# Performance work log

Hardware: AMD Instinct MI355X
Metric: run time of the kernel (lower is better)

Reference implementation:

```python
import jax, jax.numpy as jnp
import numpy as np

TARGET_SPARSITY = 0.9
LN_EPS = 1e-5


def ternary_quant(W):
    """BitNet-b1.58 style ternary quantization: W -> {-1,0,+1} * mean(|W|).
    Straight-through estimator so gradients pass to the latent weights."""
    scale = jnp.mean(jnp.abs(W))
    q = jnp.clip(jnp.round(W / (scale + 1e-8)), -1.0, 1.0) * scale
    return W + jax.lax.stop_gradient(q - W)


def layernorm(x, gamma, beta):
    mu = jnp.mean(x, axis=-1, keepdims=True)
    var = jnp.var(x, axis=-1, keepdims=True)
    return (x - mu) * jax.lax.rsqrt(var + LN_EPS) * gamma + beta


def setup_inputs() -> dict:
    key = jax.random.key(0)
    ks = jax.random.split(key, 3)
    B, S, D, N = 4, 2048, 2048, 8192
    x = jax.random.normal(ks[0], (B, S, D), dtype=jnp.float32)
    W_syn = jax.random.normal(ks[1], (N, D), dtype=jnp.float32) * (1.0 / np.sqrt(D))
    b_syn = jnp.zeros((N,), dtype=jnp.float32)
    W_out = jax.random.normal(ks[2], (D, N), dtype=jnp.float32) * (1.0 / np.sqrt(N))
    b_out = jnp.zeros((D,), dtype=jnp.float32)
    gamma = jnp.ones((D,), dtype=jnp.float32)
    beta = jnp.zeros((D,), dtype=jnp.float32)
    return {"x": x, "W_syn": W_syn, "b_syn": b_syn, "W_out": W_out,
            "b_out": b_out, "gamma": gamma, "beta": beta}


def reference(x, W_syn, b_syn, W_out, b_out, gamma, beta):
    B, S, D = x.shape
    N = W_syn.shape[0]
    x_flat = x.reshape(-1, D)  # [T, D], T = B*S

    # RNU: ternary-weight synapses + sparse firing (keep top (1-sparsity) per token)
    z = x_flat @ ternary_quant(W_syn).T + b_syn  # [T, N]
    k = max(1, int(N * (1.0 - TARGET_SPARSITY)))
    topv, _ = jax.lax.top_k(z, k)                 # [T, k]
    thresh = topv[:, -1:]                          # k-th largest per token
    hidden = jnp.where(z >= thresh, jax.nn.relu(z), 0.0)  # sparse firing rates

    # Ternary output projection
    out = hidden @ ternary_quant(W_out).T + b_out  # [T, D]
    out = out.reshape(B, S, D)

    # Residual + LayerNorm
    return layernorm(x + out, gamma, beta)
```

## Files before the change

kernel.cpp:

```cpp
#include <hip/hip_runtime.h>


typedef __attribute__((ext_vector_type(8))) short short8;
typedef __attribute__((ext_vector_type(4))) float f32x4;

__device__ __forceinline__ float bf2f(unsigned h) {
    return __uint_as_float(h << 16);
}
__device__ __forceinline__ unsigned f2bf(float f) {
    unsigned u = __float_as_uint(f);
    return (u + 0x7fffu + ((u >> 16) & 1u)) >> 16;
}

typedef __attribute__((address_space(1))) const void gq_void;
typedef __attribute__((address_space(3))) void ls_void;
__device__ __forceinline__ void gload16(const void* g, void* l) {
    __builtin_amdgcn_global_load_lds((gq_void*)g, (ls_void*)l, 16, 0, 0);
}

#define CFENCE() asm volatile("" ::: "memory")
#define BARRIER()                    \
    do {                             \
        CFENCE();                    \
        __builtin_amdgcn_s_barrier(); \
        CFENCE();                    \
    } while (0)

__global__ __launch_bounds__(64) void init_detect(float* sc, const unsigned* g_raw,
                                                  int* flag) {
    if (threadIdx.x < 16) sc[threadIdx.x] = 0.0f;
    if (threadIdx.x == 0) *flag = (g_raw[0] == 0x3F803F80u) ? 1 : 0;
}

__global__ __launch_bounds__(256) void split_x(const void* __restrict__ src,
                                               unsigned short* __restrict__ hi,
                                               unsigned short* __restrict__ lo, int n,
                                               const int* __restrict__ flagp) {
    const int flag = *flagp;
    int idx = blockIdx.x * 256 + threadIdx.x;
    int stride = gridDim.x * 256;
    if (flag) {
        const uint4* s = (const uint4*)src;
        uint4* dh = (uint4*)hi;
        uint4* dl = (uint4*)lo;
        uint4 zz; zz.x = zz.y = zz.z = zz.w = 0u;
        for (int i = idx; i < n / 8; i += stride) { dh[i] = s[i]; dl[i] = zz; }
    } else {
        const float4* s = (const float4*)src;
        uint2* dh = (uint2*)hi;
        uint2* dl = (uint2*)lo;
        for (int i = idx; i < n / 4; i += stride) {
            float4 v = s[i];
            unsigned h0 = f2bf(v.x), h1 = f2bf(v.y), h2 = f2bf(v.z), h3 = f2bf(v.w);
            unsigned l0 = f2bf(v.x - bf2f(h0));
            unsigned l1 = f2bf(v.y - bf2f(h1));
            unsigned l2 = f2bf(v.z - bf2f(h2));
            unsigned l3 = f2bf(v.w - bf2f(h3));
            uint2 oh; oh.x = h0 | (h1 << 16); oh.y = h2 | (h3 << 16);
            uint2 ol; ol.x = l0 | (l1 << 16); ol.y = l2 | (l3 << 16);
            dh[i] = oh;
            dl[i] = ol;
        }
    }
}

__global__ __launch_bounds__(256) void to_f32(const void* __restrict__ src,
                                              float* __restrict__ dst, int n,
                                              const int* __restrict__ flagp) {
    const int flag = *flagp;
    int i = blockIdx.x * 256 + threadIdx.x;
    if (i >= n) return;
    if (flag) dst[i] = bf2f((unsigned)((const unsigned short*)src)[i]);
    else dst[i] = ((const float*)src)[i];
}

__global__ __launch_bounds__(256) void abs_sum_any(const void* __restrict__ w, int n,
                                                   float* __restrict__ out,
                                                   const int* __restrict__ flagp) {
    const int flag = *flagp;
    int idx = blockIdx.x * 256 + threadIdx.x;
    int stride = gridDim.x * 256;
    float s = 0.0f;
    if (flag) {
        const uint4* wv = (const uint4*)w;
        for (int c = idx; c < n / 8; c += stride) {
            uint4 v = wv[c];
            unsigned a[4] = {v.x, v.y, v.z, v.w};
#pragma unroll
            for (int j = 0; j < 4; j++)
                s += fabsf(bf2f(a[j] & 0xffffu)) + fabsf(bf2f(a[j] >> 16));
        }
    } else {
        const float4* wv = (const float4*)w;
        for (int c = idx; c < n / 4; c += stride) {
            float4 v = wv[c];
            s += fabsf(v.x) + fabsf(v.y) + fabsf(v.z) + fabsf(v.w);
        }
    }
#pragma unroll
    for (int off = 32; off; off >>= 1) s += __shfl_down(s, off);
    __shared__ float red[4];
    int lane = threadIdx.x & 63, wv_id = threadIdx.x >> 6;
    if (lane == 0) red[wv_id] = s;
    __syncthreads();
    if (threadIdx.x == 0) atomicAdd(out, red[0] + red[1] + red[2] + red[3]);
}

__global__ __launch_bounds__(64) void finalize_scale(float* sc, float inv_count) {
    if (threadIdx.x == 0) {
        sc[2] = sc[0] * inv_count;
        sc[3] = sc[1] * inv_count;
    }
}

__global__ __launch_bounds__(256) void quantize_any(const void* __restrict__ w,
                                                    unsigned short* __restrict__ q,
                                                    const float* __restrict__ sc, int idx,
                                                    int n, const int* __restrict__ flagp) {
    const int flag = *flagp;
    const float d = sc[idx] + 1e-8f;
    int i = blockIdx.x * 256 + threadIdx.x;
    int stride = gridDim.x * 256;
    if (flag) {
        const uint4* wv = (const uint4*)w;
        uint4* qv = (uint4*)q;
        for (; i < n / 8; i += stride) {
            uint4 v = wv[i];
            unsigned a[4] = {v.x, v.y, v.z, v.w};
            unsigned r[4];
#pragma unroll
            for (int j = 0; j < 4; j++) {
                float lo = bf2f(a[j] & 0xffffu);
                float hi = bf2f(a[j] >> 16);
                float rl = fminf(1.0f, fmaxf(-1.0f, rintf(lo / d)));
                float rh = fminf(1.0f, fmaxf(-1.0f, rintf(hi / d)));
                r[j] = f2bf(rl) | (f2bf(rh) << 16);
            }
            uint4 o;
            o.x = r[0]; o.y = r[1]; o.z = r[2]; o.w = r[3];
            qv[i] = o;
        }
    } else {
        const float4* wv = (const float4*)w;
        uint2* qv = (uint2*)q;
        for (; i < n / 4; i += stride) {
            float4 v = wv[i];
            float r0 = fminf(1.0f, fmaxf(-1.0f, rintf(v.x / d)));
            float r1 = fminf(1.0f, fmaxf(-1.0f, rintf(v.y / d)));
            float r2 = fminf(1.0f, fmaxf(-1.0f, rintf(v.z / d)));
            float r3 = fminf(1.0f, fmaxf(-1.0f, rintf(v.w / d)));
            uint2 o;
            o.x = f2bf(r0) | (f2bf(r1) << 16);
            o.y = f2bf(r2) | (f2bf(r3) << 16);
            qv[i] = o;
        }
    }
}

template <bool DUAL_A>
__global__ __launch_bounds__(512, 2) void gemm8p(const unsigned short* __restrict__ A0,
                                                 const unsigned short* __restrict__ A1,
                                                 const unsigned short* __restrict__ B,
                                                 float* __restrict__ C,
                                                 const float* __restrict__ biasf,
                                                 const float* __restrict__ scp,
                                                 int scidx, int N, int K) {
    __shared__ uint4 L4[8192];

    const int tid = threadIdx.x;
    const int lane = tid & 63;
    const int wave = tid >> 6;
    const int wr = wave >> 2;
    const int wc = wave & 3;
    const int l15 = lane & 15;
    const int quad = lane >> 4;

    const int nwg = gridDim.x * gridDim.y;
    int orig = blockIdx.y * gridDim.x + blockIdx.x;
    int id = orig;
    if ((nwg & 7) == 0) id = (orig & 7) * (nwg >> 3) + (orig >> 3);
    const int bx = id % gridDim.x;
    const int by = id / gridDim.x;
    const int m0 = by * 256;
    const int n0 = bx * 256;

    f32x4 acc[8][4];
#pragma unroll
    for (int i = 0; i < 8; i++)
#pragma unroll
        for (int j = 0; j < 4; j++) acc[i][j] = (f32x4){0.f, 0.f, 0.f, 0.f};

    const unsigned short* Apan0 = A0 + (size_t)m0 * K;
    const unsigned short* Apan1 = DUAL_A ? (A1 + (size_t)m0 * K) : nullptr;
    const unsigned short* Bpan = B + (size_t)n0 * K;

    const int NT = DUAL_A ? (K >> 5) : (K >> 6);

    auto stage = [&](const unsigned short* g, int kcol, int dstChunkBase) {
#pragma unroll
        for (int i = 0; i < 2; i++) {
            int pc = tid + i * 512;
            int r = pc >> 2;
            int c4 = (pc & 3) ^ (r & 3);
            gload16(g + (size_t)r * K + kcol + c4 * 8,
                    L4 + dstChunkBase + (tid & 448) + i * 512);
        }
    };
    auto dstA = [&](int b, int s) { return (b * 2 + s) * 1024; };
    auto dstB = [&](int b, int s) { return 4096 + (b * 2 + s) * 1024; };

    auto rdA = [&](int b, int s, int R) -> short8 {
        return *(const short8*)(L4 + (b * 2 + s) * 1024 + R * 4 + (quad ^ (R & 3)));
    };
    auto rdB = [&](int b, int s, int R) -> short8 {
        return *(const short8*)(L4 + 4096 + (b * 2 + s) * 1024 + R * 4 +
                                (quad ^ (R & 3)));
    };

    stage(Apan0, 0, dstA(0, 0));
    stage(Bpan, 0, dstB(0, 0));
    stage(Apan0, 32, dstA(0, 1));
    stage(Bpan, 32, dstB(0, 1));
    asm volatile("s_waitcnt vmcnt(4)" ::: "memory");
    BARRIER();

    for (int t = 0; t < NT; ++t) {
        const int b = t & 1;
        const int bn = b ^ 1;
        const bool st = (t + 1 < NT);
        const unsigned short* Anext =
            (DUAL_A && ((t + 1) & 1)) ? Apan1 : Apan0;
        const int kbn = DUAL_A ? (((t + 1) >> 1) << 6) : ((t + 1) << 6);

        short8 a[8], b0, b1;

#pragma unroll
        for (int m = 0; m < 8; m++) a[m] = rdA(b, 0, wr * 128 + m * 16 + l15);
        b0 = rdB(b, 0, wc * 64 + 0 + l15);
        b1 = rdB(b, 0, wc * 64 + 16 + l15);
        if (st) stage(Anext, kbn + 0, dstA(bn, 0));
        BARRIER();
        __builtin_amdgcn_s_setprio(1);
#pragma unroll
        for (int m = 0; m < 8; m++) {
            acc[m][0] = __builtin_amdgcn_mfma_f32_16x16x32_bf16(a[m], b0, acc[m][0], 0, 0, 0);
            acc[m][1] = __builtin_amdgcn_mfma_f32_16x16x32_bf16(a[m], b1, acc[m][1], 0, 0, 0);
        }
        __builtin_amdgcn_s_setprio(0);
        BARRIER();

        b0 = rdB(b, 0, wc * 64 + 32 + l15);
        b1 = rdB(b, 0, wc * 64 + 48 + l15);
        if (st) {
            stage(Bpan, kbn + 0, dstB(bn, 0));
            asm volatile("s_waitcnt vmcnt(4)" ::: "memory");
        } else {
            asm volatile("s_waitcnt vmcnt(0)" ::: "memory");
        }
        BARRIER();
        __builtin_amdgcn_s_setprio(1);
#pragma unroll
        for (int m = 0; m < 8; m++) {
            acc[m][2] = __builtin_amdgcn_mfma_f32_16x16x32_bf16(a[m], b0, acc[m][2], 0, 0, 0);
            acc[m][3] = __builtin_amdgcn_mfma_f32_16x16x32_bf16(a[m], b1, acc[m][3], 0, 0, 0);
        }
        __builtin_amdgcn_s_setprio(0);
        BARRIER();

#pragma unroll
        for (int m = 0; m < 8; m++) a[m] = rdA(b, 1, wr * 128 + m * 16 + l15);
        b0 = rdB(b, 1, wc * 64 + 0 + l15);
        b1 = rdB(b, 1, wc * 64 + 16 + l15);
        if (st) stage(Anext, kbn + 32, dstA(bn, 1));
        BARRIER();
        __builtin_amdgcn_s_setprio(1);
#pragma unroll
        for (int m = 0; m < 8; m++) {
            acc[m][0] = __builtin_amdgcn_mfma_f32_16x16x32_bf16(a[m], b0, acc[m][0], 0, 0, 0);
            acc[m][1] = __builtin_amdgcn_mfma_f32_16x16x32_bf16(a[m], b1, acc[m][1], 0, 0, 0);
        }
        __builtin_amdgcn_s_setprio(0);
        BARRIER();

        b0 = rdB(b, 1, wc * 64 + 32 + l15);
        b1 = rdB(b, 1, wc * 64 + 48 + l15);
        if (st) {
            stage(Bpan, kbn + 32, dstB(bn, 1));
            asm volatile("s_waitcnt vmcnt(4)" ::: "memory");
        }
        BARRIER();
        __builtin_amdgcn_s_setprio(1);
#pragma unroll
        for (int m = 0; m < 8; m++) {
            acc[m][2] = __builtin_amdgcn_mfma_f32_16x16x32_bf16(a[m], b0, acc[m][2], 0, 0, 0);
            acc[m][3] = __builtin_amdgcn_mfma_f32_16x16x32_bf16(a[m], b1, acc[m][3], 0, 0, 0);
        }
        __builtin_amdgcn_s_setprio(0);
        BARRIER();
    }

    const float scale = scp[scidx];
#pragma unroll
    for (int n = 0; n < 4; n++) {
        int col = n0 + wc * 64 + n * 16 + l15;
        float bv = biasf[col];
#pragma unroll
        for (int m = 0; m < 8; m++) {
            int rbase = m0 + wr * 128 + m * 16 + quad * 4;
#pragma unroll
            for (int r = 0; r < 4; r++) {
                C[(size_t)(rbase + r) * N + col] = scale * acc[m][n][r] + bv;
            }
        }
    }
}

template <int BM, int BN, bool TWO>
__global__ __launch_bounds__(256) void gemm_bt_t(const unsigned short* __restrict__ A0,
                                                 const unsigned short* __restrict__ A1,
                                                 const unsigned short* __restrict__ B,
                                                 float* __restrict__ C,
                                                 const float* __restrict__ biasf,
                                                 const float* __restrict__ scp, int scidx,
                                                 int N, int K) {
    constexpr int WM = BM / 2;
    constexpr int WN = BN / 2;
    constexpr int AM = WM / 16;
    constexpr int AN = WN / 16;
    __shared__ uint4 sA[BM * 8];
    __shared__ uint4 sL[TWO ? BM * 8 : 4];
    __shared__ uint4 sB[BN * 8];
    const int tid = threadIdx.x;
    const int lane = tid & 63;
    const int wave = tid >> 6;
    const int wm = (wave >> 1) * WM;
    const int wn = (wave & 1) * WN;
    const int m0 = blockIdx.y * BM;
    const int n0 = blockIdx.x * BN;
    const int l15 = lane & 15;
    const int quad = lane >> 4;

    f32x4 acc[AM][AN];
#pragma unroll
    for (int i = 0; i < AM; i++)
#pragma unroll
        for (int j = 0; j < AN; j++) acc[i][j] = (f32x4){0.f, 0.f, 0.f, 0.f};

    const unsigned short* Abase = A0 + (size_t)m0 * K;
    const unsigned short* Lbase = TWO ? (A1 + (size_t)m0 * K) : nullptr;
    const unsigned short* Bbase = B + (size_t)n0 * K;

    for (int k0 = 0; k0 < K; k0 += 64) {
#pragma unroll
        for (int i = 0; i < BM * 8 / 256; i++) {
            int s = tid + i * 256;
            int r = s >> 3, c = s & 7;
            size_t go = (size_t)r * K + k0 + c * 8;
            gload16(Abase + go, sA + i * 256 + wave * 64);
            if (TWO) gload16(Lbase + go, sL + i * 256 + wave * 64);
        }
#pragma unroll
        for (int i = 0; i < BN * 8 / 256; i++) {
            int s = tid + i * 256;
            int r = s >> 3, c = s & 7;
            size_t go = (size_t)r * K + k0 + c * 8;
            gload16(Bbase + go, sB + i * 256 + wave * 64);
        }
        __syncthreads();
#pragma unroll
        for (int kk = 0; kk < 64; kk += 32) {
            const int jj = (kk >> 3) + quad;
            short8 ah[AM], bfr[AN];
#pragma unroll
            for (int t = 0; t < AM; t++)
                ah[t] = *(const short8*)&sA[(wm + t * 16 + l15) * 8 + jj];
#pragma unroll
            for (int t = 0; t < AN; t++)
                bfr[t] = *(const short8*)&sB[(wn + t * 16 + l15) * 8 + jj];
#pragma unroll
            for (int im = 0; im < AM; im++)
#pragma unroll
                for (int in = 0; in < AN; in++)
                    acc[im][in] = __builtin_amdgcn_mfma_f32_16x16x32_bf16(
                        ah[im], bfr[in], acc[im][in], 0, 0, 0);
            if (TWO) {
                short8 al[AM];
#pragma unroll
                for (int t = 0; t < AM; t++)
                    al[t] = *(const short8*)&sL[(wm + t * 16 + l15) * 8 + jj];
#pragma unroll
                for (int im = 0; im < AM; im++)
#pragma unroll
                    for (int in = 0; in < AN; in++)
                        acc[im][in] = __builtin_amdgcn_mfma_f32_16x16x32_bf16(
                            al[im], bfr[in], acc[im][in], 0, 0, 0);
            }
        }
        __syncthreads();
    }

    float scale = scp[scidx];
#pragma unroll
    for (int in = 0; in < AN; in++) {
        int col = n0 + wn + in * 16 + l15;
        float bv = biasf[col];
#pragma unroll
        for (int im = 0; im < AM; im++) {
            int rbase = m0 + wm + im * 16 + quad * 4;
#pragma unroll
            for (int r = 0; r < 4; r++) {
                C[(size_t)(rbase + r) * N + col] = scale * acc[im][in][r] + bv;
            }
        }
    }
}

__global__ __launch_bounds__(256) void topk_hidden(const float* __restrict__ z,
                                                   unsigned short* __restrict__ hidden,
                                                   int N, int k) {
    __shared__ unsigned keys[8192];
    __shared__ unsigned hist[2048];
    __shared__ unsigned csum[256];
    __shared__ unsigned sh_want, sh_kk;
    const int tid = threadIdx.x;
    const size_t row = blockIdx.x;
    const float* zr = z + row * (size_t)N;

    for (int i = tid; i < N; i += 256) {
        unsigned u = __float_as_uint(zr[i]);
        keys[i] = (u & 0x80000000u) ? ~u : (u | 0x80000000u);
    }
    if (tid == 0) { sh_want = 0u; sh_kk = (unsigned)k; }
    __syncthreads();

    for (int p = 0; p < 3; p++) {
        const int shift = (p == 0) ? 21 : (p == 1) ? 10 : 0;
        const int bits = (p == 2) ? 10 : 11;
        const int nb = 1 << bits;
        const unsigned want = sh_want;
        const unsigned kk = sh_kk;
        const int hs = shift + bits;
        for (int b = tid; b < nb; b += 256) hist[b] = 0u;
        __syncthreads();
        for (int i = tid; i < N; i += 256) {
            unsigned u = keys[i];
            bool match = (hs >= 32) ? true : ((u >> hs) == (want >> hs));
            if (match) atomicAdd(&hist[(u >> shift) & (nb - 1)], 1u);
        }
        __syncthreads();
        const int cs = nb >> 8;
        unsigned cv = 0;
        for (int j = 0; j < cs; j++) cv += hist[tid * cs + j];
        csum[tid] = cv;
        __syncthreads();
        for (int off = 1; off < 256; off <<= 1) {
            unsigned add = (tid + off < 256) ? csum[tid + off] : 0u;
            __syncthreads();
            csum[tid] += add;
            __syncthreads();
        }
        unsigned excl = (tid < 255) ? csum[tid + 1] : 0u;
        if (excl < kk && kk <= csum[tid]) {
            unsigned running = excl;
            for (int b = tid * cs + cs - 1; b >= tid * cs; b--) {
                unsigned h = hist[b];
                if (running + h >= kk) {
                    sh_want = want | ((unsigned)b << shift);
                    sh_kk = kk - running;
                    break;
                }
                running += h;
            }
        }
        __syncthreads();
    }

    const unsigned kth = sh_want;
    unsigned short* hr = hidden + row * (size_t)N;
    for (int i = tid; i < N; i += 256) {
        unsigned u = keys[i];
        float f = (u & 0x80000000u) ? __uint_as_float(u & 0x7fffffffu)
                                    : __uint_as_float(~u);
        float h = (u >= kth) ? fmaxf(f, 0.0f) : 0.0f;
        hr[i] = (unsigned short)f2bf(h);
    }
}

__global__ __launch_bounds__(256) void ln_kernel(const unsigned short* __restrict__ xh,
                                                 const unsigned short* __restrict__ xl,
                                                 const float* __restrict__ o,
                                                 const float* __restrict__ gamma,
                                                 const float* __restrict__ beta,
                                                 float* __restrict__ y, int D) {
    const int tid = threadIdx.x;
    const size_t row = blockIdx.x;
    const unsigned short* xhr = xh + row * (size_t)D;
    const unsigned short* xlr = xl + row * (size_t)D;
    const float* orow = o + row * (size_t)D;
    float v[8];
    float s = 0.0f, s2 = 0.0f;
#pragma unroll
    for (int j = 0; j < 8; j++) {
        int i = tid + j * 256;
        float val = bf2f((unsigned)xhr[i]) + bf2f((unsigned)xlr[i]) + orow[i];
        v[j] = val;
        s += val;
        s2 += val * val;
    }
#pragma unroll
    for (int off = 32; off; off >>= 1) {
        s += __shfl_down(s, off);
        s2 += __shfl_down(s2, off);
    }
    __shared__ float red[8];
    int lane = tid & 63, wv = tid >> 6;
    if (lane == 0) { red[wv] = s; red[4 + wv] = s2; }
    __syncthreads();
    float S = red[0] + red[1] + red[2] + red[3];
    float S2 = red[4] + red[5] + red[6] + red[7];
    float mu = S / (float)D;
    float var = S2 / (float)D - mu * mu;
    float inv = rsqrtf(var + 1e-5f);
#pragma unroll
    for (int j = 0; j < 8; j++) {
        int i = tid + j * 256;
        y[row * (size_t)D + i] = (v[j] - mu) * inv * gamma[i] + beta[i];
    }
}

extern "C" void kernel_launch(void* const* d_in, const int* in_sizes, int n_in,
                              void* d_out, int out_size, void* d_ws, size_t ws_size,
                              hipStream_t stream) {
    const void* x_raw = d_in[0];
    const void* Wsyn_raw = d_in[1];
    const void* bsyn_raw = d_in[2];
    const void* Wout_raw = d_in[3];
    const void* bout_raw = d_in[4];
    const void* gamma_raw = d_in[5];
    const void* beta_raw = d_in[6];
    float* out = (float*)d_out;

    const int M = 8192, D = 2048, N = 8192, K1 = 2048;
    const int kTop = 819;
    const int NW = M * D;

    char* wsb = (char*)d_ws;
    float* sc = (float*)wsb;
    int* flag = (int*)(wsb + 128);
    float* gamma_f = (float*)(wsb + 4096);
    float* beta_f = (float*)(wsb + 12288);
    float* bout_f = (float*)(wsb + 20480);
    float* bsyn_f = (float*)(wsb + 28672);
    unsigned short* x_hi = (unsigned short*)(wsb + 65536);
    unsigned short* x_lo = (unsigned short*)(wsb + 65536 + 1ull * 33554432ull);
    unsigned short* qsyn = (unsigned short*)(wsb + 65536 + 2ull * 33554432ull);
    unsigned short* qout = (unsigned short*)(wsb + 65536 + 3ull * 33554432ull);
    const size_t FIXED = 65536 + 4ull * 33554432ull;

    const size_t per_row = (size_t)N * 4 + (size_t)N * 2;
    size_t avail = (ws_size > FIXED) ? ws_size - FIXED : 0;
    long mc = (long)(avail / per_row);
    mc &= ~255L;
    if (mc > M) mc = M;
    if (mc < 256) mc = 256;
    const int Mc = (int)mc;
    char* chunk_base = wsb + FIXED;

    init_detect<<<1, 64, 0, stream>>>(sc, (const unsigned*)gamma_raw, flag);

    split_x<<<2048, 256, 0, stream>>>(x_raw, x_hi, x_lo, M * D, flag);
    to_f32<<<(N + 255) / 256, 256, 0, stream>>>(bsyn_raw, bsyn_f, N, flag);
    to_f32<<<(D + 255) / 256, 256, 0, stream>>>(bout_raw, bout_f, D, flag);
    to_f32<<<(D + 255) / 256, 256, 0, stream>>>(gamma_raw, gamma_f, D, flag);
    to_f32<<<(D + 255) / 256, 256, 0, stream>>>(beta_raw, beta_f, D, flag);

    abs_sum_any<<<2048, 256, 0, stream>>>(Wsyn_raw, NW, sc + 0, flag);
    abs_sum_any<<<2048, 256, 0, stream>>>(Wout_raw, NW, sc + 1, flag);
    finalize_scale<<<1, 64, 0, stream>>>(sc, 1.0f / 16777216.0f);
    quantize_any<<<2048, 256, 0, stream>>>(Wsyn_raw, qsyn, sc, 2, NW, flag);
    quantize_any<<<2048, 256, 0, stream>>>(Wout_raw, qout, sc, 3, NW, flag);

    for (int m0 = 0; m0 < M; m0 += Mc) {
        const int rows = (M - m0 < Mc) ? (M - m0) : Mc;
        float* z = (float*)chunk_base;
        unsigned short* hidden = (unsigned short*)(chunk_base + (size_t)Mc * N * 4);
        float* outf = (float*)chunk_base;

        dim3 g1(N / 256, rows / 256);
        gemm8p<true><<<g1, 512, 0, stream>>>(x_hi + (size_t)m0 * K1,
                                             x_lo + (size_t)m0 * K1, qsyn, z, bsyn_f,
                                             sc, 2, N, K1);

        topk_hidden<<<rows, 256, 0, stream>>>(z, hidden, N, kTop);

        dim3 g2(D / 64, rows / 128);
        gemm_bt_t<128, 64, false><<<g2, 256, 0, stream>>>(hidden, nullptr, qout, outf,
                                                          bout_f, sc, 3, D, N);

        ln_kernel<<<rows, 256, 0, stream>>>(x_hi + (size_t)m0 * D, x_lo + (size_t)m0 * D,
                                            outf, gamma_f, beta_f, out + (size_t)m0 * D,
                                            D);
    }
}
```

Baseline: 2.047 ms.

## Deepen GEMM prefetch pipeline and reorder K-loop for dual-A split

Restructures the GEMM main loop so global-to-LDS loads run one and a half stages ahead, keeping up to eight loads in flight instead of four. The dual-A (hi/lo split) path now walks all K tiles of the high part and then all tiles of the low part, instead of interleaving them per tile. The workgroup-id swizzle is also changed to walk tiles column-major after the modulo-8 remap, which changes L2 reuse across neighbouring workgroups. The aim is to hide more global memory latency behind the MFMA work, at the cost of more complex waitcnt bookkeeping near the end of the loop.

```diff
diff --git a/kernel.cpp b/kernel.cpp
--- a/kernel.cpp
+++ b/kernel.cpp
@@ -19,11 +19,11 @@
 }
 
 #define CFENCE() asm volatile("" ::: "memory")
-#define BARRIER()                    \
-    do {                             \
-        CFENCE();                    \
+#define BARRIER()                     \
+    do {                              \
+        CFENCE();                     \
         __builtin_amdgcn_s_barrier(); \
-        CFENCE();                    \
+        CFENCE();                     \
     } while (0)
 
 __global__ __launch_bounds__(64) void init_detect(float* sc, const unsigned* g_raw,
@@ -157,7 +157,7 @@
     }
 }
 
-template <bool DUAL_A>
+template <bool DUAL>
 __global__ __launch_bounds__(512, 2) void gemm8p(const unsigned short* __restrict__ A0,
                                                  const unsigned short* __restrict__ A1,
                                                  const unsigned short* __restrict__ B,
@@ -175,12 +175,18 @@
     const int l15 = lane & 15;
     const int quad = lane >> 4;
 
-    const int nwg = gridDim.x * gridDim.y;
-    int orig = blockIdx.y * gridDim.x + blockIdx.x;
-    int id = orig;
-    if ((nwg & 7) == 0) id = (orig & 7) * (nwg >> 3) + (orig >> 3);
-    const int bx = id % gridDim.x;
-    const int by = id / gridDim.x;
+    const int GX = gridDim.x, GY = gridDim.y;
+    const int nwg = GX * GY;
+    int orig = blockIdx.y * GX + blockIdx.x;
+    int bx, by;
+    if ((nwg & 7) == 0) {
+        int id = (orig & 7) * (nwg >> 3) + (orig >> 3);
+        bx = id / GY;
+        by = id - bx * GY;
+    } else {
+        bx = blockIdx.x;
+        by = blockIdx.y;
+    }
     const int m0 = by * 256;
     const int n0 = bx * 256;
 
@@ -190,55 +196,51 @@
 #pragma unroll
         for (int j = 0; j < 4; j++) acc[i][j] = (f32x4){0.f, 0.f, 0.f, 0.f};
 
-    const unsigned short* Apan0 = A0 + (size_t)m0 * K;
-    const unsigned short* Apan1 = DUAL_A ? (A1 + (size_t)m0 * K) : nullptr;
-    const unsigned short* Bpan = B + (size_t)n0 * K;
-
-    const int NT = DUAL_A ? (K >> 5) : (K >> 6);
-
-    auto stage = [&](const unsigned short* g, int kcol, int dstChunkBase) {
+    const unsigned short* Ah = A0 + (size_t)m0 * K;
+    const unsigned short* Al = DUAL ? (A1 + (size_t)m0 * K) : nullptr;
+    const unsigned short* Bp = B + (size_t)n0 * K;
+
+    const int NTH = K >> 6;
+    const int NT = DUAL ? 2 * NTH : NTH;
+
+    auto stage = [&](int mat, int T, int s) {
+        if (T >= NT) return;
+        const unsigned short* g = mat ? Bp : ((DUAL && T >= NTH) ? Al : Ah);
+        const int kcol = ((DUAL && T >= NTH) ? (T - NTH) : T) * 64 + s * 32;
+        const int dstBase = (mat ? 4096 : 0) + (((T & 1) * 2 + s) << 10);
 #pragma unroll
         for (int i = 0; i < 2; i++) {
             int pc = tid + i * 512;
             int r = pc >> 2;
             int c4 = (pc & 3) ^ (r & 3);
             gload16(g + (size_t)r * K + kcol + c4 * 8,
-                    L4 + dstChunkBase + (tid & 448) + i * 512);
+                    L4 + dstBase + (tid & 448) + i * 512);
         }
     };
-    auto dstA = [&](int b, int s) { return (b * 2 + s) * 1024; };
-    auto dstB = [&](int b, int s) { return 4096 + (b * 2 + s) * 1024; };
 
     auto rdA = [&](int b, int s, int R) -> short8 {
-        return *(const short8*)(L4 + (b * 2 + s) * 1024 + R * 4 + (quad ^ (R & 3)));
+        return *(const short8*)(L4 + ((b * 2 + s) << 10) + R * 4 + (quad ^ (R & 3)));
     };
     auto rdB = [&](int b, int s, int R) -> short8 {
-        return *(const short8*)(L4 + 4096 + (b * 2 + s) * 1024 + R * 4 +
+        return *(const short8*)(L4 + 4096 + ((b * 2 + s) << 10) + R * 4 +
                                 (quad ^ (R & 3)));
     };
 
-    stage(Apan0, 0, dstA(0, 0));
-    stage(Bpan, 0, dstB(0, 0));
-    stage(Apan0, 32, dstA(0, 1));
-    stage(Bpan, 32, dstB(0, 1));
-    asm volatile("s_waitcnt vmcnt(4)" ::: "memory");
+    stage(0, 0, 0); stage(1, 0, 0);
+    stage(0, 0, 1); stage(1, 0, 1);
+    stage(0, 1, 0); stage(1, 1, 0);
+    asm volatile("s_waitcnt vmcnt(8)" ::: "memory");
     BARRIER();
 
-    for (int t = 0; t < NT; ++t) {
-        const int b = t & 1;
-        const int bn = b ^ 1;
-        const bool st = (t + 1 < NT);
-        const unsigned short* Anext =
-            (DUAL_A && ((t + 1) & 1)) ? Apan1 : Apan0;
-        const int kbn = DUAL_A ? (((t + 1) >> 1) << 6) : ((t + 1) << 6);
-
+    for (int T = 0; T < NT; ++T) {
+        const int b = T & 1;
         short8 a[8], b0, b1;
 
 #pragma unroll
         for (int m = 0; m < 8; m++) a[m] = rdA(b, 0, wr * 128 + m * 16 + l15);
         b0 = rdB(b, 0, wc * 64 + 0 + l15);
         b1 = rdB(b, 0, wc * 64 + 16 + l15);
-        if (st) stage(Anext, kbn + 0, dstA(bn, 0));
+        stage(0, T + 1, 1);
         BARRIER();
         __builtin_amdgcn_s_setprio(1);
 #pragma unroll
@@ -251,12 +253,9 @@
 
         b0 = rdB(b, 0, wc * 64 + 32 + l15);
         b1 = rdB(b, 0, wc * 64 + 48 + l15);
-        if (st) {
-            stage(Bpan, kbn + 0, dstB(bn, 0));
-            asm volatile("s_waitcnt vmcnt(4)" ::: "memory");
-        } else {
-            asm volatile("s_waitcnt vmcnt(0)" ::: "memory");
-        }
+        stage(1, T + 1, 1);
+        if (T == NT - 1) asm volatile("s_waitcnt vmcnt(0)" ::: "memory");
+        else             asm volatile("s_waitcnt vmcnt(8)" ::: "memory");
         BARRIER();
         __builtin_amdgcn_s_setprio(1);
 #pragma unroll
@@ -271,7 +270,7 @@
         for (int m = 0; m < 8; m++) a[m] = rdA(b, 1, wr * 128 + m * 16 + l15);
         b0 = rdB(b, 1, wc * 64 + 0 + l15);
         b1 = rdB(b, 1, wc * 64 + 16 + l15);
-        if (st) stage(Anext, kbn + 32, dstA(bn, 1));
+        stage(0, T + 2, 0);
         BARRIER();
         __builtin_amdgcn_s_setprio(1);
 #pragma unroll
@@ -284,9 +283,10 @@
 
         b0 = rdB(b, 1, wc * 64 + 32 + l15);
         b1 = rdB(b, 1, wc * 64 + 48 + l15);
-        if (st) {
-            stage(Bpan, kbn + 32, dstB(bn, 1));
-            asm volatile("s_waitcnt vmcnt(4)" ::: "memory");
+        stage(1, T + 2, 0);
+        if (T < NT - 1) {
+            if (T == NT - 2) asm volatile("s_waitcnt vmcnt(4)" ::: "memory");
+            else             asm volatile("s_waitcnt vmcnt(8)" ::: "memory");
         }
         BARRIER();
         __builtin_amdgcn_s_setprio(1);
```

Result: no change. 2.059 ms (+0.6%).
